# Performance work log

Measured on AMD Instinct MI355X. Metric: run time of the kernel, lower is better.

## Reference

```python
import jax, jax.numpy as jnp
import numpy as np

B, S, K = 2, 256, 2          # batch, seq, banks_selected (top-k)
IN, OUT, NB = 512, 512, 16   # in_features, out_features, num_banks


def setup_inputs() -> dict:
    key = jax.random.key(0)
    k1, k2, k3, k4 = jax.random.split(key, 4)
    bound = 1.0 / np.sqrt(IN)  # nn.Linear default init range
    tensor = jax.random.normal(k1, (B, S, K, IN), dtype=jnp.float32)
    bank_selections = jax.random.randint(k2, (B, S, K), 0, NB)
    # stacked nn.Linear params: weight (num_banks, out, in), bias (num_banks, out)
    weight = jax.random.uniform(k3, (NB, OUT, IN), dtype=jnp.float32, minval=-bound, maxval=bound)
    bias = jax.random.uniform(k4, (NB, OUT), dtype=jnp.float32, minval=-bound, maxval=bound)
    return {"tensor": tensor, "bank_selections": bank_selections, "weight": weight, "bias": bias}


def reference(tensor, bank_selections, weight, bias):
    # Gather per-selection weights/bias, exactly as extract_weights/extract_bias.
    w_sel = weight[bank_selections]  # (B, S, K, OUT, IN) -- the large expanded intermediate
    b_sel = bias[bank_selections]    # (B, S, K, OUT)
    # Per-selection linear: out[..., k, :] = x[..., k, :] @ W[sel[..., k]].T + b[sel[..., k]]
    return jnp.einsum('bski,bskoi->bsko', tensor, w_sel) + b_sel
```

## Files before the change

kernel.cpp:

```cpp
#include <hip/hip_runtime.h>

#define NB   16
#define INF  512
#define OUTF 512

typedef __attribute__((ext_vector_type(8))) short bf16x8;
typedef __attribute__((ext_vector_type(4))) float f32x4;

static __device__ __forceinline__ ushort f2bf(float f) {
    unsigned u = __float_as_uint(f);
    u += 0x7FFFu + ((u >> 16) & 1u);
    return (ushort)(u >> 16);
}

__global__ __launch_bounds__(256) void prep_kernel(
    const float* __restrict__ x, const int* __restrict__ sel,
    const float* __restrict__ W,
    int* __restrict__ counts, int* __restrict__ lists,
    ushort* __restrict__ xb, ushort* __restrict__ Wb, int nrows)
{
    int t = threadIdx.x;
    if (blockIdx.x == 0) {
        __shared__ int cnt[NB];
        if (t < NB) cnt[t] = 0;
        __syncthreads();
        for (int r = t; r < nrows; r += 256) {
            int b = sel[r];
            int pos = atomicAdd(&cnt[b], 1);
            lists[b * nrows + pos] = r;
        }
        __syncthreads();
        if (t < NB) counts[t] = cnt[t];
        return;
    }
    const int nvw = NB * OUTF * INF / 4;
    const int nvx = (nrows * INF) / 4;
    int gid = (blockIdx.x - 1) * 256 + t;
    int stride = (gridDim.x - 1) * 256;
    const float4* Wf = (const float4*)W;
    const float4* xf = (const float4*)x;
    ushort4* Wo = (ushort4*)Wb;
    ushort4* xo = (ushort4*)xb;
    for (int i = gid; i < nvw + nvx; i += stride) {
        if (i < nvw) {
            float4 v = Wf[i];
            ushort4 o;
            o.x = f2bf(v.x); o.y = f2bf(v.y); o.z = f2bf(v.z); o.w = f2bf(v.w);
            Wo[i] = o;
        } else {
            int j = i - nvw;
            float4 v = xf[j];
            ushort4 o;
            o.x = f2bf(v.x); o.y = f2bf(v.y); o.z = f2bf(v.z); o.w = f2bf(v.w);
            xo[j] = o;
        }
    }
}

__global__ __launch_bounds__(256) void mfma_gemm(
    const ushort* __restrict__ xb, const ushort* __restrict__ Wb,
    const float* __restrict__ bias, const int* __restrict__ counts,
    const int* __restrict__ lists, float* __restrict__ out, int nrows_total)
{
    int bank = blockIdx.z;
    int nrows = counts[bank];
    int row0 = blockIdx.y * 16;
    if (row0 >= nrows) return;

    __shared__ int ridx[16];
    int t = threadIdx.x;
    if (t < 16) {
        int r = row0 + t;
        ridx[t] = lists[bank * nrows_total + ((r < nrows) ? r : 0)];
    }
    __syncthreads();

    int lane = t & 63;
    int wave = t >> 6;
    int ln = lane & 15;
    int q  = lane >> 4;

    int o_glob = blockIdx.x * 64 + wave * 16 + ln;
    const ushort* ap = xb + (size_t)ridx[ln] * INF + q * 8;
    const ushort* bp = Wb + ((size_t)bank * OUTF + o_glob) * INF + q * 8;

    f32x4 acc = {0.f, 0.f, 0.f, 0.f};
#pragma unroll 4
    for (int k = 0; k < INF; k += 32) {
        bf16x8 a = *(const bf16x8*)ap; ap += 32;
        bf16x8 b = *(const bf16x8*)bp; bp += 32;
        acc = __builtin_amdgcn_mfma_f32_16x16x32_bf16(a, b, acc, 0, 0, 0);
    }

    float bv = bias[bank * OUTF + o_glob];
#pragma unroll
    for (int r = 0; r < 4; ++r) {
        int m = q * 4 + r;
        if (row0 + m < nrows)
            out[(size_t)ridx[m] * OUTF + o_glob] = acc[r] + bv;
    }
}

extern "C" void kernel_launch(void* const* d_in, const int* in_sizes, int n_in,
                              void* d_out, int out_size, void* d_ws, size_t ws_size,
                              hipStream_t stream) {
    const float* tensor = (const float*)d_in[0];
    const int*   sel    = (const int*)d_in[1];
    const float* weight = (const float*)d_in[2];
    const float* bias   = (const float*)d_in[3];
    float* out = (float*)d_out;

    int nrows = in_sizes[1];

    int* counts = (int*)d_ws;
    int* lists  = counts + NB;
    size_t int_bytes = (size_t)(NB + NB * nrows) * sizeof(int);
    size_t xb_bytes  = (size_t)nrows * INF * sizeof(ushort);
    ushort* xb = (ushort*)((char*)d_ws + int_bytes);
    ushort* Wb = (ushort*)((char*)d_ws + int_bytes + xb_bytes);

    prep_kernel<<<1025, 256, 0, stream>>>(tensor, sel, weight, counts, lists,
                                          xb, Wb, nrows);
    dim3 grid(OUTF / 64, (nrows + 15) / 16, NB);
    mfma_gemm<<<grid, 256, 0, stream>>>(xb, Wb, bias, counts, lists, out, nrows);
}
```

Measured before the change: 104.4 us.

## Fuse routing, bf16 conversion and banked GEMM into one kernel

Replaces the two-kernel scheme (a prep kernel that builds per-bank row lists and writes bf16 copies of all weights and inputs, then an MFMA GEMM) with one fused kernel. Each block owns one bank and 16 output features. It builds that bank's row list in shared memory by scanning the selections, converts its weight slice to bf16 straight into registers, and loops over 16-row tiles across waves, converting x on the fly. This removes the full-weight bf16 write and reread plus a kernel launch. In exchange, x rows are read and converted once per output-slice block, and any bank with more than 256 selected rows would silently drop rows.

```diff
diff --git a/kernel.cpp b/kernel.cpp
--- a/kernel.cpp
+++ b/kernel.cpp
@@ -3,6 +3,7 @@
 #define NB   16
 #define INF  512
 #define OUTF 512
+#define MAXR 256
 
 typedef __attribute__((ext_vector_type(8))) short bf16x8;
 typedef __attribute__((ext_vector_type(4))) float f32x4;
@@ -13,91 +14,72 @@
     return (ushort)(u >> 16);
 }
 
-__global__ __launch_bounds__(256) void prep_kernel(
+static __device__ __forceinline__ bf16x8 cvt8(const float* __restrict__ p) {
+    float4 v0 = *(const float4*)p;
+    float4 v1 = *(const float4*)(p + 4);
+    bf16x8 r;
+    r[0] = (short)f2bf(v0.x); r[1] = (short)f2bf(v0.y);
+    r[2] = (short)f2bf(v0.z); r[3] = (short)f2bf(v0.w);
+    r[4] = (short)f2bf(v1.x); r[5] = (short)f2bf(v1.y);
+    r[6] = (short)f2bf(v1.z); r[7] = (short)f2bf(v1.w);
+    return r;
+}
+
+__global__ __launch_bounds__(256) void fused_banked(
     const float* __restrict__ x, const int* __restrict__ sel,
-    const float* __restrict__ W,
-    int* __restrict__ counts, int* __restrict__ lists,
-    ushort* __restrict__ xb, ushort* __restrict__ Wb, int nrows)
+    const float* __restrict__ W, const float* __restrict__ bias,
+    float* __restrict__ out, int nrows)
 {
+    int bank = blockIdx.y;
+    int o0 = blockIdx.x * 16;
+
+    __shared__ int lst[MAXR];
+    __shared__ int cnt_s;
     int t = threadIdx.x;
-    if (blockIdx.x == 0) {
-        __shared__ int cnt[NB];
-        if (t < NB) cnt[t] = 0;
-        __syncthreads();
-        for (int r = t; r < nrows; r += 256) {
-            int b = sel[r];
-            int pos = atomicAdd(&cnt[b], 1);
-            lists[b * nrows + pos] = r;
-        }
-        __syncthreads();
-        if (t < NB) counts[t] = cnt[t];
-        return;
-    }
-    const int nvw = NB * OUTF * INF / 4;
-    const int nvx = (nrows * INF) / 4;
-    int gid = (blockIdx.x - 1) * 256 + t;
-    int stride = (gridDim.x - 1) * 256;
-    const float4* Wf = (const float4*)W;
-    const float4* xf = (const float4*)x;
-    ushort4* Wo = (ushort4*)Wb;
-    ushort4* xo = (ushort4*)xb;
-    for (int i = gid; i < nvw + nvx; i += stride) {
-        if (i < nvw) {
-            float4 v = Wf[i];
-            ushort4 o;
-            o.x = f2bf(v.x); o.y = f2bf(v.y); o.z = f2bf(v.z); o.w = f2bf(v.w);
-            Wo[i] = o;
-        } else {
-            int j = i - nvw;
-            float4 v = xf[j];
-            ushort4 o;
-            o.x = f2bf(v.x); o.y = f2bf(v.y); o.z = f2bf(v.z); o.w = f2bf(v.w);
-            xo[j] = o;
+    if (t == 0) cnt_s = 0;
+    __syncthreads();
+    for (int r = t; r < nrows; r += 256) {
+        if (sel[r] == bank) {
+            int pos = atomicAdd(&cnt_s, 1);
+            if (pos < MAXR) lst[pos] = r;
         }
     }
-}
-
-__global__ __launch_bounds__(256) void mfma_gemm(
-    const ushort* __restrict__ xb, const ushort* __restrict__ Wb,
-    const float* __restrict__ bias, const int* __restrict__ counts,
-    const int* __restrict__ lists, float* __restrict__ out, int nrows_total)
-{
-    int bank = blockIdx.z;
-    int nrows = counts[bank];
-    int row0 = blockIdx.y * 16;
-    if (row0 >= nrows) return;
-
-    __shared__ int ridx[16];
-    int t = threadIdx.x;
-    if (t < 16) {
-        int r = row0 + t;
-        ridx[t] = lists[bank * nrows_total + ((r < nrows) ? r : 0)];
-    }
     __syncthreads();
+    int c = cnt_s;
+    if (c > MAXR) c = MAXR;
+    int ntiles = (c + 15) >> 4;
 
     int lane = t & 63;
     int wave = t >> 6;
     int ln = lane & 15;
     int q  = lane >> 4;
 
-    int o_glob = blockIdx.x * 64 + wave * 16 + ln;
-    const ushort* ap = xb + (size_t)ridx[ln] * INF + q * 8;
-    const ushort* bp = Wb + ((size_t)bank * OUTF + o_glob) * INF + q * 8;
+    const float* wrow = W + ((size_t)bank * OUTF + o0 + ln) * INF + q * 8;
+    bf16x8 bfr[16];
+#pragma unroll
+    for (int i = 0; i < 16; ++i) bfr[i] = cvt8(wrow + i * 32);
 
-    f32x4 acc = {0.f, 0.f, 0.f, 0.f};
-#pragma unroll 4
-    for (int k = 0; k < INF; k += 32) {
-        bf16x8 a = *(const bf16x8*)ap; ap += 32;
-        bf16x8 b = *(const bf16x8*)bp; bp += 32;
-        acc = __builtin_amdgcn_mfma_f32_16x16x32_bf16(a, b, acc, 0, 0, 0);
-    }
+    float bv = bias[bank * OUTF + o0 + ln];
 
-    float bv = bias[bank * OUTF + o_glob];
+    for (int T = wave; T < ntiles; T += 4) {
+        int row0 = T * 16;
+        int rl = row0 + ln;
+        int rg = lst[rl < c ? rl : 0];
+        const float* ap = x + (size_t)rg * INF + q * 8;
+
+        f32x4 acc = {0.f, 0.f, 0.f, 0.f};
 #pragma unroll
-    for (int r = 0; r < 4; ++r) {
-        int m = q * 4 + r;
-        if (row0 + m < nrows)
-            out[(size_t)ridx[m] * OUTF + o_glob] = acc[r] + bv;
+        for (int i = 0; i < 16; ++i) {
+            bf16x8 a = cvt8(ap + i * 32);
+            acc = __builtin_amdgcn_mfma_f32_16x16x32_bf16(a, bfr[i], acc, 0, 0, 0);
+        }
+
+#pragma unroll
+        for (int r = 0; r < 4; ++r) {
+            int m = q * 4 + r;
+            if (row0 + m < c)
+                out[(size_t)lst[row0 + m] * OUTF + o0 + ln] = acc[r] + bv;
+        }
     }
 }
 
@@ -112,15 +94,6 @@
 
     int nrows = in_sizes[1];
 
-    int* counts = (int*)d_ws;
-    int* lists  = counts + NB;
-    size_t int_bytes = (size_t)(NB + NB * nrows) * sizeof(int);
-    size_t xb_bytes  = (size_t)nrows * INF * sizeof(ushort);
-    ushort* xb = (ushort*)((char*)d_ws + int_bytes);
-    ushort* Wb = (ushort*)((char*)d_ws + int_bytes + xb_bytes);
-
-    prep_kernel<<<1025, 256, 0, stream>>>(tensor, sel, weight, counts, lists,
-                                          xb, Wb, nrows);
-    dim3 grid(OUTF / 64, (nrows + 15) / 16, NB);
-    mfma_gemm<<<grid, 256, 0, stream>>>(xb, Wb, bias, counts, lists, out, nrows);
+    dim3 grid(OUTF / 16, NB, 1);
+    fused_banked<<<grid, 256, 0, stream>>>(tensor, sel, weight, bias, out, nrows);
 }
```

Result: faster. 91.14 us (-12.7%).

## Schedule GEMM over a compacted tile list instead of a dense bank grid

Applied to the files above, without the earlier changes.

The prep kernel now builds a packed list of (bank, row offset, row count) tiles from the per-bank counts. The GEMM grid covers only that bounded list of tiles instead of a dense grid over every bank and the worst-case row range, where most blocks exited immediately. The GEMM also drops the shared-memory row index and barrier in favour of a cross-lane shuffle, and splits the K loop across two accumulators to expose more MFMA parallelism. Adding the tile list puts serial work on one thread in the prep kernel, and the cost of converting the weights is unchanged.

```diff
diff --git a/kernel.cpp b/kernel.cpp
--- a/kernel.cpp
+++ b/kernel.cpp
@@ -3,6 +3,7 @@
 #define NB   16
 #define INF  512
 #define OUTF 512
+#define MAXT 80
 
 typedef __attribute__((ext_vector_type(8))) short bf16x8;
 typedef __attribute__((ext_vector_type(4))) float f32x4;
@@ -13,10 +14,12 @@
     return (ushort)(u >> 16);
 }
 
+#define HDR_INTS (MAXT)
+
 __global__ __launch_bounds__(256) void prep_kernel(
     const float* __restrict__ x, const int* __restrict__ sel,
     const float* __restrict__ W,
-    int* __restrict__ counts, int* __restrict__ lists,
+    int* __restrict__ tiles, int* __restrict__ lists,
     ushort* __restrict__ xb, ushort* __restrict__ Wb, int nrows)
 {
     int t = threadIdx.x;
@@ -30,7 +33,18 @@
             lists[b * nrows + pos] = r;
         }
         __syncthreads();
-        if (t < NB) counts[t] = cnt[t];
+        if (t == 0) {
+            if (cnt[0] == 0) lists[0] = 0;
+            int nt = 0;
+            for (int b = 0; b < NB; ++b) {
+                int c = cnt[b];
+                for (int r0 = 0; r0 < c; r0 += 16) {
+                    int m = c - r0; if (m > 16) m = 16;
+                    tiles[nt++] = (b << 20) | (r0 << 8) | m;
+                }
+            }
+            for (; nt < MAXT; ++nt) tiles[nt] = 0;
+        }
         return;
     }
     const int nvw = NB * OUTF * INF / 4;
@@ -59,45 +73,45 @@
 
 __global__ __launch_bounds__(256) void mfma_gemm(
     const ushort* __restrict__ xb, const ushort* __restrict__ Wb,
-    const float* __restrict__ bias, const int* __restrict__ counts,
+    const float* __restrict__ bias, const int* __restrict__ tiles,
     const int* __restrict__ lists, float* __restrict__ out, int nrows_total)
 {
-    int bank = blockIdx.z;
-    int nrows = counts[bank];
-    int row0 = blockIdx.y * 16;
-    if (row0 >= nrows) return;
+    int tb = tiles[blockIdx.y];
+    int mrows = tb & 0xff;
+    if (mrows == 0) return;
+    int bank = tb >> 20;
+    int row0 = (tb >> 8) & 0xfff;
 
-    __shared__ int ridx[16];
-    int t = threadIdx.x;
-    if (t < 16) {
-        int r = row0 + t;
-        ridx[t] = lists[bank * nrows_total + ((r < nrows) ? r : 0)];
-    }
-    __syncthreads();
-
-    int lane = t & 63;
-    int wave = t >> 6;
+    int lane = threadIdx.x & 63;
+    int wave = threadIdx.x >> 6;
     int ln = lane & 15;
     int q  = lane >> 4;
 
-    int o_glob = blockIdx.x * 64 + wave * 16 + ln;
-    const ushort* ap = xb + (size_t)ridx[ln] * INF + q * 8;
-    const ushort* bp = Wb + ((size_t)bank * OUTF + o_glob) * INF + q * 8;
+    int o = blockIdx.x * 64 + wave * 16 + ln;
+    int rg = lists[bank * nrows_total + row0 + (ln < mrows ? ln : 0)];
+    float bv = bias[bank * OUTF + o];
 
-    f32x4 acc = {0.f, 0.f, 0.f, 0.f};
-#pragma unroll 4
-    for (int k = 0; k < INF; k += 32) {
-        bf16x8 a = *(const bf16x8*)ap; ap += 32;
-        bf16x8 b = *(const bf16x8*)bp; bp += 32;
-        acc = __builtin_amdgcn_mfma_f32_16x16x32_bf16(a, b, acc, 0, 0, 0);
+    const ushort* ap = xb + (size_t)rg * INF + q * 8;
+    const ushort* bp = Wb + ((size_t)bank * OUTF + o) * INF + q * 8;
+
+    f32x4 acc0 = {0.f, 0.f, 0.f, 0.f};
+    f32x4 acc1 = {0.f, 0.f, 0.f, 0.f};
+#pragma unroll
+    for (int i = 0; i < 8; ++i) {
+        bf16x8 a0 = *(const bf16x8*)(ap + (2 * i) * 32);
+        bf16x8 b0 = *(const bf16x8*)(bp + (2 * i) * 32);
+        bf16x8 a1 = *(const bf16x8*)(ap + (2 * i + 1) * 32);
+        bf16x8 b1 = *(const bf16x8*)(bp + (2 * i + 1) * 32);
+        acc0 = __builtin_amdgcn_mfma_f32_16x16x32_bf16(a0, b0, acc0, 0, 0, 0);
+        acc1 = __builtin_amdgcn_mfma_f32_16x16x32_bf16(a1, b1, acc1, 0, 0, 0);
     }
 
-    float bv = bias[bank * OUTF + o_glob];
 #pragma unroll
     for (int r = 0; r < 4; ++r) {
         int m = q * 4 + r;
-        if (row0 + m < nrows)
-            out[(size_t)ridx[m] * OUTF + o_glob] = acc[r] + bv;
+        int rowg = __shfl(rg, m, 16);
+        if (m < mrows)
+            out[(size_t)rowg * OUTF + o] = acc0[r] + acc1[r] + bv;
     }
 }
 
@@ -112,15 +126,15 @@
 
     int nrows = in_sizes[1];
 
-    int* counts = (int*)d_ws;
-    int* lists  = counts + NB;
-    size_t int_bytes = (size_t)(NB + NB * nrows) * sizeof(int);
+    int* tiles = (int*)d_ws;
+    int* lists = tiles + HDR_INTS;
+    size_t int_bytes = (size_t)(HDR_INTS + NB * nrows) * sizeof(int);
     size_t xb_bytes  = (size_t)nrows * INF * sizeof(ushort);
     ushort* xb = (ushort*)((char*)d_ws + int_bytes);
     ushort* Wb = (ushort*)((char*)d_ws + int_bytes + xb_bytes);
 
-    prep_kernel<<<1025, 256, 0, stream>>>(tensor, sel, weight, counts, lists,
+    prep_kernel<<<1025, 256, 0, stream>>>(tensor, sel, weight, tiles, lists,
                                           xb, Wb, nrows);
-    dim3 grid(OUTF / 64, (nrows + 15) / 16, NB);
-    mfma_gemm<<<grid, 256, 0, stream>>>(xb, Wb, bias, counts, lists, out, nrows);
+    dim3 grid(OUTF / 64, MAXT, 1);
+    mfma_gemm<<<grid, 256, 0, stream>>>(xb, Wb, bias, tiles, lists, out, nrows);
 }
```

After: 87.66 us, median of 2. -16.1%, faster.
